# Optimization experiments

Measured on AMD Instinct MI355X. Metric: run time of the kernel, lower is better.

Reference implementation:

```python
import jax, jax.numpy as jnp
import numpy as np

B, H, W, C = 4, 64, 64, 128
NHEADS = 2

def setup_inputs() -> dict:
    key = jax.random.key(0)
    k1, k2, k3 = jax.random.split(key, 3)
    x = jax.random.normal(k1, (B, H, W, C), dtype=jnp.float32)
    # 1x1 conv weights (flax Conv kernel (1,1,Cin,Cout) squeezed to [Cin,Cout])
    w_qkv = jax.random.normal(k2, (C, 3 * C), dtype=jnp.float32) * (C ** -0.5)
    w_out = jax.random.normal(k3, (C, C), dtype=jnp.float32) * (C ** -0.5)
    b_out = jnp.zeros((C,), dtype=jnp.float32)
    return {"x": x, "w_qkv": w_qkv, "w_out": w_out, "b_out": b_out}

def reference(x, w_qkv, w_out, b_out):
    b, h, w, c = x.shape
    n_heads = NHEADS
    head_c = c // n_heads
    scale = c ** (-0.5)  # NOTE: original scales by n_channels**-0.5 (not head_c)
    # 1x1 conv == per-pixel matmul
    qkv = jnp.einsum('bhwc,cd->bhwd', x, w_qkv)
    qkv = qkv.reshape(b, h * w, n_heads, 3 * head_c)
    q, k, v = jnp.split(qkv, 3, axis=-1)  # each [b, N, heads, head_c]
    atten = jnp.einsum('bihd,bjhd->bijh', q, k) * scale  # [b, N, N, heads]
    atten = jax.nn.softmax(atten, axis=2)
    res = jnp.einsum('bijh,bjhd->bihd', atten, v)  # [b, N, heads, head_c]
    res = res.reshape(b, h, w, n_heads * head_c)
    out = jnp.einsum('bhwc,cd->bhwd', res, w_out) + b_out
    return out
```

## Files before the change

### kernel.cpp

```cpp
#include <hip/hip_runtime.h>
#include <hip/hip_bf16.h>

#define NT 4096
#define HD 64
#define CCH 128
#define LOG2E 1.4426950408889634f
#define QK_SCALE 0.08838834764831845f
#define QSCALE_LOG2 (QK_SCALE * LOG2E)

typedef __attribute__((ext_vector_type(8))) short short8;
typedef __attribute__((ext_vector_type(4))) float f32x4;

__device__ __forceinline__ float4 ld4(const float* p) {
    return *reinterpret_cast<const float4*>(p);
}

__device__ __forceinline__ unsigned short f2bf(float f) {
    union { float f; unsigned u; } v; v.f = f;
    unsigned r = v.u + 0x7fff + ((v.u >> 16) & 1);
    return (unsigned short)(r >> 16);
}

__device__ __forceinline__ unsigned pkbf(float a, float b) {
    __hip_bfloat162 h = __float22bfloat162_rn(make_float2(a, b));
    return *reinterpret_cast<unsigned*>(&h);
}

__device__ __forceinline__ float exp2fast(float x) {
#if __has_builtin(__builtin_amdgcn_exp2f)
    return __builtin_amdgcn_exp2f(x);
#else
    return exp2f(x);
#endif
}

__global__ __launch_bounds__(256) void k_qkv(const float* __restrict__ x,
                                             const float* __restrict__ wqkv,
                                             unsigned short* __restrict__ Qb,
                                             unsigned short* __restrict__ Kb,
                                             unsigned short* __restrict__ Vt) {
    __shared__ __align__(16) unsigned short xs[64][128];
    __shared__ __align__(16) unsigned short wt[64][128];
    const int t  = threadIdx.x;
    const int mt = blockIdx.x;
    const int nt = blockIdx.y;

    {
        const int r = t >> 2, qd = t & 3;
        const float* src = &x[(size_t)(mt * 64 + r) * CCH + qd * 32];
        unsigned pk[16];
        #pragma unroll
        for (int i = 0; i < 8; ++i) {
            float4 v = ld4(src + i * 4);
            pk[2 * i]     = pkbf(v.x, v.y);
            pk[2 * i + 1] = pkbf(v.z, v.w);
        }
        #pragma unroll
        for (int g2 = 0; g2 < 4; ++g2) {
            const int gp = (qd * 4 + g2) ^ (r & 7);
            *reinterpret_cast<uint4*>(&xs[r][gp * 8]) =
                make_uint4(pk[4 * g2], pk[4 * g2 + 1], pk[4 * g2 + 2], pk[4 * g2 + 3]);
        }
    }
    {
        const int g  = t >> 4;
        const int j4 = (t & 15) * 4;
        float4 col[8];
        #pragma unroll
        for (int kk = 0; kk < 8; ++kk)
            col[kk] = ld4(&wqkv[(size_t)(g * 8 + kk) * 384 + nt * 64 + j4]);
        const float* c = reinterpret_cast<const float*>(col);
        #pragma unroll
        for (int jj = 0; jj < 4; ++jj) {
            const int j = j4 + jj;
            unsigned a0 = pkbf(c[0 * 4 + jj], c[1 * 4 + jj]);
            unsigned a1 = pkbf(c[2 * 4 + jj], c[3 * 4 + jj]);
            unsigned a2 = pkbf(c[4 * 4 + jj], c[5 * 4 + jj]);
            unsigned a3 = pkbf(c[6 * 4 + jj], c[7 * 4 + jj]);
            *reinterpret_cast<uint4*>(&wt[j][(g ^ (j & 7)) * 8]) = make_uint4(a0, a1, a2, a3);
        }
    }
    __syncthreads();

    const int lane = t & 63, w = t >> 6, q = lane & 15, Lw = lane >> 4;

    short8 qa4[4];
    #pragma unroll
    for (int ks = 0; ks < 4; ++ks)
        qa4[ks] = *reinterpret_cast<const short8*>(
            &xs[w * 16 + q][((Lw + 4 * ks) ^ (q & 7)) * 8]);

    f32x4 acc[4];
    #pragma unroll
    for (int ct = 0; ct < 4; ++ct) acc[ct] = (f32x4)0.f;
    #pragma unroll
    for (int ct = 0; ct < 4; ++ct) {
        const int j = ct * 16 + q;
        #pragma unroll
        for (int ks = 0; ks < 4; ++ks) {
            short8 wb = *reinterpret_cast<const short8*>(
                &wt[j][((Lw + 4 * ks) ^ (j & 7)) * 8]);
            acc[ct] = __builtin_amdgcn_mfma_f32_16x16x32_bf16(qa4[ks], wb, acc[ct], 0, 0, 0);
        }
    }

    const int head  = nt / 3;
    const int which = nt - 3 * head;
    const int gi0 = mt * 64 + w * 16 + Lw * 4;
    const int bb  = gi0 >> 12;
    const int n0  = gi0 & 4095;
    const int bhh = bb * 2 + head;

    if (which == 0) {
        #pragma unroll
        for (int ct = 0; ct < 4; ++ct) {
            const int d = ct * 16 + q;
            #pragma unroll
            for (int r = 0; r < 4; ++r)
                Qb[((size_t)(bhh * NT + n0 + r)) * HD + d] = f2bf(acc[ct][r] * QSCALE_LOG2);
        }
    } else if (which == 1) {
        #pragma unroll
        for (int ct = 0; ct < 4; ++ct) {
            const int d = ct * 16 + q;
            #pragma unroll
            for (int r = 0; r < 4; ++r)
                Kb[((size_t)(bhh * NT + n0 + r)) * HD + d] = f2bf(acc[ct][r]);
        }
    } else {
        #pragma unroll
        for (int ct = 0; ct < 4; ++ct) {
            const int d = ct * 16 + q;
            uint2 u;
            u.x = pkbf(acc[ct][0], acc[ct][1]);
            u.y = pkbf(acc[ct][2], acc[ct][3]);
            *reinterpret_cast<uint2*>(&Vt[((size_t)(bhh * HD + d)) * NT + n0]) = u;
        }
    }
}

__global__ __launch_bounds__(256) void k_attn(const unsigned short* __restrict__ Qb,
                                              const unsigned short* __restrict__ Kb,
                                              const unsigned short* __restrict__ Vt,
                                              float* __restrict__ R) {
    __shared__ __align__(16) char smem[41984];
    char* Ks0 = smem;
    char* Ks1 = smem + 8192;
    char* Vs0 = smem + 16384;
    char* Vs1 = smem + 24576;
    char* PwA = smem + 32768;

    const int t    = threadIdx.x;
    const int lane = t & 63;
    const int w    = t >> 6;
    const int qt   = blockIdx.x;
    const int bh   = blockIdx.y;

    const char* KbT = (const char*)Kb + (size_t)bh * NT * HD * 2;
    const char* VtT = (const char*)Vt + (size_t)bh * HD * NT * 2;

    const int q  = lane & 15;
    const int Lw = lane >> 4;

    short8 qa[2];
    {
        const int qrow = qt * 64 + w * 16 + q;
        const char* qp = (const char*)Qb +
            (((size_t)bh * NT + qrow) * HD + (Lw * 8)) * 2;
        qa[0] = *reinterpret_cast<const short8*>(qp);
        qa[1] = *reinterpret_cast<const short8*>(qp + 64);
    }

    char* Prow = PwA + w * 2304 + q * 144;

    float mrow = -1e30f, lrow = 0.f;
    f32x4 oacc[4];
    #pragma unroll
    for (int i = 0; i < 4; ++i) oacc[i] = (f32x4)0.f;

    const int rc0 = t >> 3;
    const int sp  = t & 7;
    const int rc1 = rc0 + 32;

    const char* kp0 = KbT + rc0 * 128 + (sp ^ (rc0 & 7)) * 16;
    const char* kp1 = KbT + rc1 * 128 + (sp ^ (rc1 & 7)) * 16;
    const char* vp0 = VtT + (size_t)rc0 * 8192 + (sp ^ (rc0 & 7)) * 16;
    const char* vp1 = VtT + (size_t)rc1 * 8192 + (sp ^ (rc1 & 7)) * 16;

    auto gll = [](const char* g, char* l) {
        __builtin_amdgcn_global_load_lds(
            (const __attribute__((address_space(1))) void*)g,
            (__attribute__((address_space(3))) void*)l, 16, 0, 0);
    };
    auto stage = [&](char* KsD, char* VsD) {
        gll(kp0, KsD + t * 16); gll(kp1, KsD + 4096 + t * 16);
        gll(vp0, VsD + t * 16); gll(vp1, VsD + 4096 + t * 16);
        kp0 += 8192; kp1 += 8192; vp0 += 128; vp1 += 128;
    };

    auto compute = [&](const char* KsC, const char* VsC) {
        f32x4 sacc[4];
        #pragma unroll
        for (int ct = 0; ct < 4; ++ct) sacc[ct] = (f32x4)0.f;
        #pragma unroll
        for (int ct = 0; ct < 4; ++ct) {
            const int j = ct * 16 + q;
            #pragma unroll
            for (int ks = 0; ks < 2; ++ks) {
                const int slot = (Lw + 4 * ks) ^ (lane & 7);
                short8 kb = *reinterpret_cast<const short8*>(KsC + j * 128 + slot * 16);
                sacc[ct] = __builtin_amdgcn_mfma_f32_16x16x32_bf16(kb, qa[ks], sacc[ct], 0, 0, 0);
            }
        }
        float mx = -1e30f;
        #pragma unroll
        for (int ct = 0; ct < 4; ++ct)
            #pragma unroll
            for (int r = 0; r < 4; ++r) mx = fmaxf(mx, sacc[ct][r]);
        mx = fmaxf(mx, __shfl_xor(mx, 16));
        mx = fmaxf(mx, __shfl_xor(mx, 32));
        const float mn = fmaxf(mrow, mx);
        const float corr = exp2fast(mrow - mn);
        mrow = mn;
        float e[4][4];
        float sum = 0.f;
        #pragma unroll
        for (int ct = 0; ct < 4; ++ct)
            #pragma unroll
            for (int r = 0; r < 4; ++r) {
                float ev = exp2fast(sacc[ct][r] - mn);
                e[ct][r] = ev;
                sum += ev;
            }
        sum += __shfl_xor(sum, 16);
        sum += __shfl_xor(sum, 32);
        lrow = lrow * corr + sum;
        #pragma unroll
        for (int dt = 0; dt < 4; ++dt) oacc[dt] *= corr;

        #pragma unroll
        for (int ct = 0; ct < 4; ++ct) {
            const int g = 2 * ct + (Lw >> 1);
            uint2 u = make_uint2(pkbf(e[ct][0], e[ct][1]), pkbf(e[ct][2], e[ct][3]));
            *reinterpret_cast<uint2*>(Prow + (((g + 2 * q) & 7) << 4) + ((Lw & 1) << 3)) = u;
        }
        short8 pb[2];
        #pragma unroll
        for (int ks = 0; ks < 2; ++ks)
            pb[ks] = *reinterpret_cast<const short8*>(
                Prow + (((Lw + 4 * ks + 2 * q) & 7) << 4));

        #pragma unroll
        for (int dt = 0; dt < 4; ++dt) {
            const int d = dt * 16 + q;
            #pragma unroll
            for (int ks = 0; ks < 2; ++ks) {
                const int slot = (Lw + 4 * ks) ^ (lane & 7);
                short8 vb = *reinterpret_cast<const short8*>(VsC + d * 128 + slot * 16);
                oacc[dt] = __builtin_amdgcn_mfma_f32_16x16x32_bf16(vb, pb[ks], oacc[dt], 0, 0, 0);
            }
        }
    };

    stage(Ks0, Vs0);
    __syncthreads();
    for (int it = 0; it < 32; ++it) {
        stage(Ks1, Vs1);
        compute(Ks0, Vs0);
        __syncthreads();
        if (it < 31) stage(Ks0, Vs0);
        compute(Ks1, Vs1);
        __syncthreads();
    }

    const int b = bh >> 1, h = bh & 1;
    const float inv = 1.0f / lrow;
    const int row = qt * 64 + w * 16 + q;
    float* dst = &R[((size_t)(b * NT + row)) * CCH + h * HD];
    #pragma unroll
    for (int dt = 0; dt < 4; ++dt) {
        float4 v = make_float4(oacc[dt][0] * inv, oacc[dt][1] * inv,
                               oacc[dt][2] * inv, oacc[dt][3] * inv);
        *reinterpret_cast<float4*>(&dst[dt * 16 + Lw * 4]) = v;
    }
}

__global__ __launch_bounds__(256) void k_out(const float* __restrict__ R,
                                             const float* __restrict__ wout,
                                             const float* __restrict__ bout,
                                             float* __restrict__ out) {
    __shared__ float xs[64][132];
    __shared__ float ws[128][68];
    const int t  = threadIdx.x;
    const int mt = blockIdx.x;
    const int nt = blockIdx.y;

    #pragma unroll
    for (int f = 0; f < 8; ++f) {
        int g = f * 256 + t;
        int r = g >> 5, c = (g & 31) << 2;
        *reinterpret_cast<float4*>(&xs[r][c]) = ld4(&R[(mt * 64 + r) * CCH + c]);
    }
    #pragma unroll
    for (int f = 0; f < 8; ++f) {
        int g = f * 256 + t;
        int r = g >> 4, c = (g & 15) << 2;
        *reinterpret_cast<float4*>(&ws[r][c]) = ld4(&wout[r * CCH + nt * 64 + c]);
    }
    __syncthreads();

    const int r0 = (t >> 4) << 2;
    const int c0 = (t & 15) << 2;
    float acc[4][4] = {};
    #pragma unroll 8
    for (int k4 = 0; k4 < 32; ++k4) {
        float a[4][4], b[4][4];
        #pragma unroll
        for (int i = 0; i < 4; ++i) {
            float4 v = ld4(&xs[r0 + i][k4 * 4]);
            a[i][0] = v.x; a[i][1] = v.y; a[i][2] = v.z; a[i][3] = v.w;
        }
        #pragma unroll
        for (int kk = 0; kk < 4; ++kk) {
            float4 v = ld4(&ws[k4 * 4 + kk][c0]);
            b[kk][0] = v.x; b[kk][1] = v.y; b[kk][2] = v.z; b[kk][3] = v.w;
        }
        #pragma unroll
        for (int i = 0; i < 4; ++i)
            #pragma unroll
            for (int kk = 0; kk < 4; ++kk)
                #pragma unroll
                for (int j = 0; j < 4; ++j)
                    acc[i][j] += a[i][kk] * b[kk][j];
    }

    float4 bias = ld4(&bout[nt * 64 + c0]);
    #pragma unroll
    for (int i = 0; i < 4; ++i) {
        int gi = mt * 64 + r0 + i;
        float4 v = make_float4(acc[i][0] + bias.x, acc[i][1] + bias.y,
                               acc[i][2] + bias.z, acc[i][3] + bias.w);
        *reinterpret_cast<float4*>(&out[(size_t)gi * CCH + nt * 64 + c0]) = v;
    }
}

extern "C" void kernel_launch(void* const* d_in, const int* in_sizes, int n_in,
                              void* d_out, int out_size, void* d_ws, size_t ws_size,
                              hipStream_t stream) {
    const float* x    = (const float*)d_in[0];
    const float* wqkv = (const float*)d_in[1];
    const float* wout = (const float*)d_in[2];
    const float* bout = (const float*)d_in[3];
    float* out = (float*)d_out;

    unsigned short* Qb = (unsigned short*)d_ws;
    unsigned short* Kb = Qb + 2097152;
    unsigned short* Vt = Kb + 2097152;
    float* R = (float*)((char*)d_ws + 12 * 1024 * 1024);

    k_qkv<<<dim3(256, 6), 256, 0, stream>>>(x, wqkv, Qb, Kb, Vt);
    k_attn<<<dim3(64, 8), 256, 0, stream>>>(Qb, Kb, Vt, R);
    k_out<<<dim3(256, 2), 256, 0, stream>>>(R, wout, bout, out);
}
```

Baseline: 162.5 us.

## Split KV columns across wave pairs and skip rescale with lazy max threshold

```diff
diff --git a/kernel.cpp b/kernel.cpp
--- a/kernel.cpp
+++ b/kernel.cpp
@@ -143,7 +143,7 @@
                                               const unsigned short* __restrict__ Kb,
                                               const unsigned short* __restrict__ Vt,
                                               float* __restrict__ R) {
-    __shared__ __align__(16) char smem[41984];
+    __shared__ __align__(16) char smem[37888];
     char* Ks0 = smem;
     char* Ks1 = smem + 8192;
     char* Vs0 = smem + 16384;
@@ -153,6 +153,8 @@
     const int t    = threadIdx.x;
     const int lane = t & 63;
     const int w    = t >> 6;
+    const int rh   = w >> 1;
+    const int p    = w & 1;
     const int qt   = blockIdx.x;
     const int bh   = blockIdx.y;
 
@@ -164,14 +166,14 @@
 
     short8 qa[2];
     {
-        const int qrow = qt * 64 + w * 16 + q;
+        const int qrow = qt * 32 + rh * 16 + q;
         const char* qp = (const char*)Qb +
             (((size_t)bh * NT + qrow) * HD + (Lw * 8)) * 2;
         qa[0] = *reinterpret_cast<const short8*>(qp);
         qa[1] = *reinterpret_cast<const short8*>(qp + 64);
     }
 
-    char* Prow = PwA + w * 2304 + q * 144;
+    char* Prow = PwA + w * 1280 + q * 80;
 
     float mrow = -1e30f, lrow = 0.f;
     f32x4 oacc[4];
@@ -199,66 +201,61 @@
     };
 
     auto compute = [&](const char* KsC, const char* VsC) {
-        f32x4 sacc[4];
-        #pragma unroll
-        for (int ct = 0; ct < 4; ++ct) sacc[ct] = (f32x4)0.f;
-        #pragma unroll
-        for (int ct = 0; ct < 4; ++ct) {
-            const int j = ct * 16 + q;
+        f32x4 sacc[2];
+        sacc[0] = (f32x4)0.f; sacc[1] = (f32x4)0.f;
+        #pragma unroll
+        for (int c = 0; c < 2; ++c) {
+            const int j = (2 * p + c) * 16 + q;
             #pragma unroll
             for (int ks = 0; ks < 2; ++ks) {
                 const int slot = (Lw + 4 * ks) ^ (lane & 7);
                 short8 kb = *reinterpret_cast<const short8*>(KsC + j * 128 + slot * 16);
-                sacc[ct] = __builtin_amdgcn_mfma_f32_16x16x32_bf16(kb, qa[ks], sacc[ct], 0, 0, 0);
+                sacc[c] = __builtin_amdgcn_mfma_f32_16x16x32_bf16(kb, qa[ks], sacc[c], 0, 0, 0);
             }
         }
         float mx = -1e30f;
         #pragma unroll
-        for (int ct = 0; ct < 4; ++ct)
-            #pragma unroll
-            for (int r = 0; r < 4; ++r) mx = fmaxf(mx, sacc[ct][r]);
+        for (int c = 0; c < 2; ++c)
+            #pragma unroll
+            for (int r = 0; r < 4; ++r) mx = fmaxf(mx, sacc[c][r]);
         mx = fmaxf(mx, __shfl_xor(mx, 16));
         mx = fmaxf(mx, __shfl_xor(mx, 32));
-        const float mn = fmaxf(mrow, mx);
-        const float corr = exp2fast(mrow - mn);
-        mrow = mn;
-        float e[4][4];
+        if (!__all(mx <= mrow + 8.0f)) {
+            const float mn = fmaxf(mrow, mx);
+            const float corr = exp2fast(mrow - mn);
+            mrow = mn;
+            lrow *= corr;
+            #pragma unroll
+            for (int dt = 0; dt < 4; ++dt) oacc[dt] *= corr;
+        }
+        float e[2][4];
         float sum = 0.f;
         #pragma unroll
-        for (int ct = 0; ct < 4; ++ct)
+        for (int c = 0; c < 2; ++c)
             #pragma unroll
             for (int r = 0; r < 4; ++r) {
-                float ev = exp2fast(sacc[ct][r] - mn);
-                e[ct][r] = ev;
+                float ev = exp2fast(sacc[c][r] - mrow);
+                e[c][r] = ev;
                 sum += ev;
             }
         sum += __shfl_xor(sum, 16);
         sum += __shfl_xor(sum, 32);
-        lrow = lrow * corr + sum;
-        #pragma unroll
-        for (int dt = 0; dt < 4; ++dt) oacc[dt] *= corr;
-
-        #pragma unroll
-        for (int ct = 0; ct < 4; ++ct) {
-            const int g = 2 * ct + (Lw >> 1);
-            uint2 u = make_uint2(pkbf(e[ct][0], e[ct][1]), pkbf(e[ct][2], e[ct][3]));
-            *reinterpret_cast<uint2*>(Prow + (((g + 2 * q) & 7) << 4) + ((Lw & 1) << 3)) = u;
-        }
-        short8 pb[2];
-        #pragma unroll
-        for (int ks = 0; ks < 2; ++ks)
-            pb[ks] = *reinterpret_cast<const short8*>(
-                Prow + (((Lw + 4 * ks + 2 * q) & 7) << 4));
+        lrow += sum;
+
+        #pragma unroll
+        for (int c = 0; c < 2; ++c) {
+            const int g = 2 * c + (Lw >> 1);
+            uint2 u = make_uint2(pkbf(e[c][0], e[c][1]), pkbf(e[c][2], e[c][3]));
+            *reinterpret_cast<uint2*>(Prow + (((g + q) & 3) << 4) + ((Lw & 1) << 3)) = u;
+        }
+        short8 pb = *reinterpret_cast<const short8*>(Prow + (((Lw + q) & 3) << 4));
 
         #pragma unroll
         for (int dt = 0; dt < 4; ++dt) {
             const int d = dt * 16 + q;
-            #pragma unroll
-            for (int ks = 0; ks < 2; ++ks) {
-                const int slot = (Lw + 4 * ks) ^ (lane & 7);
-                short8 vb = *reinterpret_cast<const short8*>(VsC + d * 128 + slot * 16);
-                oacc[dt] = __builtin_amdgcn_mfma_f32_16x16x32_bf16(vb, pb[ks], oacc[dt], 0, 0, 0);
-            }
+            const int slot = (4 * p + Lw) ^ (lane & 7);
+            short8 vb = *reinterpret_cast<const short8*>(VsC + d * 128 + slot * 16);
+            oacc[dt] = __builtin_amdgcn_mfma_f32_16x16x32_bf16(vb, pb, oacc[dt], 0, 0, 0);
         }
     };
 
@@ -273,15 +270,34 @@
         __syncthreads();
     }
 
-    const int b = bh >> 1, h = bh & 1;
-    const float inv = 1.0f / lrow;
-    const int row = qt * 64 + w * 16 + q;
-    float* dst = &R[((size_t)(b * NT + row)) * CCH + h * HD];
-    #pragma unroll
-    for (int dt = 0; dt < 4; ++dt) {
-        float4 v = make_float4(oacc[dt][0] * inv, oacc[dt][1] * inv,
-                               oacc[dt][2] * inv, oacc[dt][3] * inv);
-        *reinterpret_cast<float4*>(&dst[dt * 16 + Lw * 4]) = v;
+    if (p) {
+        float* dst = reinterpret_cast<float*>(smem) + (rh * 64 + lane) * 18;
+        #pragma unroll
+        for (int dt = 0; dt < 4; ++dt)
+            #pragma unroll
+            for (int r = 0; r < 4; ++r) dst[dt * 4 + r] = oacc[dt][r];
+        dst[16] = mrow; dst[17] = lrow;
+    }
+    __syncthreads();
+    if (!p) {
+        const float* src = reinterpret_cast<const float*>(smem) + (rh * 64 + lane) * 18;
+        const float m1 = src[16], l1 = src[17];
+        const float m  = fmaxf(mrow, m1);
+        const float c0 = exp2fast(mrow - m);
+        const float c1 = exp2fast(m1 - m);
+        const float inv = 1.0f / (lrow * c0 + l1 * c1);
+        const int b = bh >> 1, h = bh & 1;
+        const int row = qt * 32 + rh * 16 + q;
+        float* dst = &R[((size_t)(b * NT + row)) * CCH + h * HD];
+        #pragma unroll
+        for (int dt = 0; dt < 4; ++dt) {
+            float4 v;
+            v.x = (oacc[dt][0] * c0 + src[dt * 4 + 0] * c1) * inv;
+            v.y = (oacc[dt][1] * c0 + src[dt * 4 + 1] * c1) * inv;
+            v.z = (oacc[dt][2] * c0 + src[dt * 4 + 2] * c1) * inv;
+            v.w = (oacc[dt][3] * c0 + src[dt * 4 + 3] * c1) * inv;
+            *reinterpret_cast<float4*>(&dst[dt * 16 + Lw * 4]) = v;
+        }
     }
 }
 
@@ -359,6 +375,6 @@
     float* R = (float*)((char*)d_ws + 12 * 1024 * 1024);
 
     k_qkv<<<dim3(256, 6), 256, 0, stream>>>(x, wqkv, Qb, Kb, Vt);
-    k_attn<<<dim3(64, 8), 256, 0, stream>>>(Qb, Kb, Vt, R);
+    k_attn<<<dim3(128, 8), 256, 0, stream>>>(Qb, Kb, Vt, R);
     k_out<<<dim3(256, 2), 256, 0, stream>>>(R, wout, bout, out);
 }
```

After: 174.6 us. 1.07x slower.

## Store attention output as bf16 and run output projection with MFMA

Applied to the files above, without the earlier changes.

```diff
diff --git a/kernel.cpp b/kernel.cpp
--- a/kernel.cpp
+++ b/kernel.cpp
@@ -142,7 +142,7 @@
 __global__ __launch_bounds__(256) void k_attn(const unsigned short* __restrict__ Qb,
                                               const unsigned short* __restrict__ Kb,
                                               const unsigned short* __restrict__ Vt,
-                                              float* __restrict__ R) {
+                                              unsigned short* __restrict__ Rb) {
     __shared__ __align__(16) char smem[41984];
     char* Ks0 = smem;
     char* Ks1 = smem + 8192;
@@ -276,71 +276,78 @@
     const int b = bh >> 1, h = bh & 1;
     const float inv = 1.0f / lrow;
     const int row = qt * 64 + w * 16 + q;
-    float* dst = &R[((size_t)(b * NT + row)) * CCH + h * HD];
+    unsigned short* dst = &Rb[((size_t)(b * NT + row)) * CCH + h * HD];
     #pragma unroll
     for (int dt = 0; dt < 4; ++dt) {
-        float4 v = make_float4(oacc[dt][0] * inv, oacc[dt][1] * inv,
-                               oacc[dt][2] * inv, oacc[dt][3] * inv);
-        *reinterpret_cast<float4*>(&dst[dt * 16 + Lw * 4]) = v;
-    }
-}
-
-__global__ __launch_bounds__(256) void k_out(const float* __restrict__ R,
+        uint2 u;
+        u.x = pkbf(oacc[dt][0] * inv, oacc[dt][1] * inv);
+        u.y = pkbf(oacc[dt][2] * inv, oacc[dt][3] * inv);
+        *reinterpret_cast<uint2*>(&dst[dt * 16 + Lw * 4]) = u;
+    }
+}
+
+__global__ __launch_bounds__(256) void k_out(const unsigned short* __restrict__ Rb,
                                              const float* __restrict__ wout,
                                              const float* __restrict__ bout,
                                              float* __restrict__ out) {
-    __shared__ float xs[64][132];
-    __shared__ float ws[128][68];
+    __shared__ __align__(16) unsigned short wt[64][128];
     const int t  = threadIdx.x;
     const int mt = blockIdx.x;
     const int nt = blockIdx.y;
 
-    #pragma unroll
-    for (int f = 0; f < 8; ++f) {
-        int g = f * 256 + t;
-        int r = g >> 5, c = (g & 31) << 2;
-        *reinterpret_cast<float4*>(&xs[r][c]) = ld4(&R[(mt * 64 + r) * CCH + c]);
-    }
-    #pragma unroll
-    for (int f = 0; f < 8; ++f) {
-        int g = f * 256 + t;
-        int r = g >> 4, c = (g & 15) << 2;
-        *reinterpret_cast<float4*>(&ws[r][c]) = ld4(&wout[r * CCH + nt * 64 + c]);
+    {
+        const int g  = t >> 4;
+        const int j4 = (t & 15) * 4;
+        float4 col[8];
+        #pragma unroll
+        for (int kk = 0; kk < 8; ++kk)
+            col[kk] = ld4(&wout[(size_t)(g * 8 + kk) * CCH + nt * 64 + j4]);
+        const float* c = reinterpret_cast<const float*>(col);
+        #pragma unroll
+        for (int jj = 0; jj < 4; ++jj) {
+            const int j = j4 + jj;
+            unsigned a0 = pkbf(c[0 * 4 + jj], c[1 * 4 + jj]);
+            unsigned a1 = pkbf(c[2 * 4 + jj], c[3 * 4 + jj]);
+            unsigned a2 = pkbf(c[4 * 4 + jj], c[5 * 4 + jj]);
+            unsigned a3 = pkbf(c[6 * 4 + jj], c[7 * 4 + jj]);
+            *reinterpret_cast<uint4*>(&wt[j][(g ^ (j & 7)) * 8]) = make_uint4(a0, a1, a2, a3);
+        }
+    }
+
+    const int lane = t & 63, w = t >> 6, q = lane & 15, Lw = lane >> 4;
+
+    short8 ra[4];
+    {
+        const char* rp = (const char*)Rb +
+            (((size_t)(mt * 64 + w * 16 + q)) * CCH + Lw * 8) * 2;
+        #pragma unroll
+        for (int ks = 0; ks < 4; ++ks)
+            ra[ks] = *reinterpret_cast<const short8*>(rp + ks * 64);
     }
     __syncthreads();
 
-    const int r0 = (t >> 4) << 2;
-    const int c0 = (t & 15) << 2;
-    float acc[4][4] = {};
-    #pragma unroll 8
-    for (int k4 = 0; k4 < 32; ++k4) {
-        float a[4][4], b[4][4];
-        #pragma unroll
-        for (int i = 0; i < 4; ++i) {
-            float4 v = ld4(&xs[r0 + i][k4 * 4]);
-            a[i][0] = v.x; a[i][1] = v.y; a[i][2] = v.z; a[i][3] = v.w;
-        }
-        #pragma unroll
-        for (int kk = 0; kk < 4; ++kk) {
-            float4 v = ld4(&ws[k4 * 4 + kk][c0]);
-            b[kk][0] = v.x; b[kk][1] = v.y; b[kk][2] = v.z; b[kk][3] = v.w;
-        }
-        #pragma unroll
-        for (int i = 0; i < 4; ++i)
-            #pragma unroll
-            for (int kk = 0; kk < 4; ++kk)
-                #pragma unroll
-                for (int j = 0; j < 4; ++j)
-                    acc[i][j] += a[i][kk] * b[kk][j];
-    }
-
-    float4 bias = ld4(&bout[nt * 64 + c0]);
-    #pragma unroll
-    for (int i = 0; i < 4; ++i) {
-        int gi = mt * 64 + r0 + i;
-        float4 v = make_float4(acc[i][0] + bias.x, acc[i][1] + bias.y,
-                               acc[i][2] + bias.z, acc[i][3] + bias.w);
-        *reinterpret_cast<float4*>(&out[(size_t)gi * CCH + nt * 64 + c0]) = v;
+    f32x4 acc[4];
+    #pragma unroll
+    for (int ct = 0; ct < 4; ++ct) acc[ct] = (f32x4)0.f;
+    #pragma unroll
+    for (int ct = 0; ct < 4; ++ct) {
+        const int j = ct * 16 + q;
+        #pragma unroll
+        for (int ks = 0; ks < 4; ++ks) {
+            short8 wb = *reinterpret_cast<const short8*>(
+                &wt[j][((Lw + 4 * ks) ^ (j & 7)) * 8]);
+            acc[ct] = __builtin_amdgcn_mfma_f32_16x16x32_bf16(ra[ks], wb, acc[ct], 0, 0, 0);
+        }
+    }
+
+    const int row0 = mt * 64 + w * 16 + Lw * 4;
+    #pragma unroll
+    for (int ct = 0; ct < 4; ++ct) {
+        const int col = nt * 64 + ct * 16 + q;
+        const float bias = bout[col];
+        #pragma unroll
+        for (int r = 0; r < 4; ++r)
+            out[(size_t)(row0 + r) * CCH + col] = acc[ct][r] + bias;
     }
 }
 
@@ -356,9 +363,9 @@
     unsigned short* Qb = (unsigned short*)d_ws;
     unsigned short* Kb = Qb + 2097152;
     unsigned short* Vt = Kb + 2097152;
-    float* R = (float*)((char*)d_ws + 12 * 1024 * 1024);
+    unsigned short* Rb = Vt + 2097152;
 
     k_qkv<<<dim3(256, 6), 256, 0, stream>>>(x, wqkv, Qb, Kb, Vt);
-    k_attn<<<dim3(64, 8), 256, 0, stream>>>(Qb, Kb, Vt, R);
-    k_out<<<dim3(256, 2), 256, 0, stream>>>(R, wout, bout, out);
-}
+    k_attn<<<dim3(64, 8), 256, 0, stream>>>(Qb, Kb, Vt, Rb);
+    k_out<<<dim3(256, 2), 256, 0, stream>>>(Rb, wout, bout, out);
+}
```

Result: faster. 152.2 us (-6.4%).
